# Performance work log

Measured on AMD Instinct MI355X. Metric: run time of the kernel, lower is better.

The kernel has to match this reference:

```python
import jax, jax.numpy as jnp
import numpy as np

N, E, H = 2000, 4096, 256

def setup_inputs() -> dict:
    key = jax.random.key(0)
    ks = jax.random.split(key, 24)
    def rn(k, shape, scale=0.05):
        return jax.random.normal(k, shape, dtype=jnp.float32) * scale
    inp = {
        'x': jax.random.randint(ks[0], (N, 1), 0, 5),
        'pos': rn(ks[1], (N, 3), 1.0),
        'edge_index': jax.random.randint(ks[2], (2, E), 0, N),
        'edge_atr': rn(ks[3], (E, 5), 1.0),
        'emb_table': rn(ks[4], (5, 5), 1.0),
        'lin0_W': rn(ks[5], (H, 8)), 'lin0_b': jnp.zeros((H,), jnp.float32),
        'mlp1_W': rn(ks[6], (128, 5)), 'mlp1_b': jnp.zeros((128,), jnp.float32),
        'mlp2_W': rn(ks[7], (H * H, 128), 0.01), 'mlp2_b': jnp.zeros((H * H,), jnp.float32),
        'conv_b': jnp.zeros((H,), jnp.float32),
        'gru_Wih': rn(ks[8], (3 * H, H)), 'gru_Whh': rn(ks[9], (3 * H, H)),
        'gru_bih': jnp.zeros((3 * H,), jnp.float32), 'gru_bhh': jnp.zeros((3 * H,), jnp.float32),
        'lin1_W': rn(ks[10], (H, 2 * H)), 'lin1_b': jnp.zeros((H,), jnp.float32),
        'lin2_W': rn(ks[11], (242, H)), 'lin2_b': jnp.zeros((242,), jnp.float32),
        'l6_W1': rn(ks[12], (128, 2 * H)), 'l6_b1': jnp.zeros((128,), jnp.float32),
        'bn_g': jnp.ones((128,), jnp.float32), 'bn_b': jnp.zeros((128,), jnp.float32),
        'l6_W2': rn(ks[13], (1, 128)), 'l6_b2': jnp.zeros((1,), jnp.float32),
    }
    return inp

def _gru_step(m, h, Wih, Whh, bih, bhh):
    gi = m @ Wih.T + bih  # [N,3H]
    gh = h @ Whh.T + bhh
    gir, giz, gin = jnp.split(gi, 3, axis=1)
    ghr, ghz, ghn = jnp.split(gh, 3, axis=1)
    r = jax.nn.sigmoid(gir + ghr)
    z = jax.nn.sigmoid(giz + ghz)
    n = jnp.tanh(gin + r * ghn)
    return (1.0 - z) * n + z * h

def reference(x, pos, edge_index, edge_atr, emb_table, lin0_W, lin0_b,
              mlp1_W, mlp1_b, mlp2_W, mlp2_b, conv_b,
              gru_Wih, gru_Whh, gru_bih, gru_bhh,
              lin1_W, lin1_b, lin2_W, lin2_b,
              l6_W1, l6_b1, bn_g, bn_b, l6_W2, l6_b2):
    node_emb = emb_table[x[:, 0]]                      # [N,5]
    in_p = jnp.concatenate([node_emb, pos], axis=1)    # [N,8]
    out = jax.nn.relu(in_p @ lin0_W.T + lin0_b)        # [N,H]
    h = out
    row, col = edge_index[0], edge_index[1]
    # edge-conditioned weights (edge_atr is loop-invariant -> compute once)
    he = jax.nn.relu(edge_atr @ mlp1_W.T + mlp1_b)     # [E,128]
    W_e = (he @ mlp2_W.T + mlp2_b).reshape(E, H, H)    # [E,H,H]
    counts = jnp.clip(jax.ops.segment_sum(jnp.ones((E,), jnp.float32), col, num_segments=N), 1.0)
    for _ in range(3):
        msg = jnp.einsum('eh,eho->eo', out[row], W_e)  # gather + per-edge matmul
        agg = jax.ops.segment_sum(msg, col, num_segments=N) / counts[:, None] + conv_b
        m = jax.nn.relu(agg)
        h = _gru_step(m, h, gru_Wih, gru_Whh, gru_bih, gru_bhh)
        out = h
    out_concat = jnp.concatenate([out[row], out[col]], axis=1)  # [E,2H]
    o1 = jax.nn.relu(out_concat @ lin1_W.T + lin1_b)
    out2 = o1 @ lin2_W.T + lin2_b                       # [E,242]
    # lin6: Linear -> BatchNorm1d (batch stats, training mode) -> ReLU -> Linear
    h1 = out_concat @ l6_W1.T + l6_b1                   # [E,128]
    mu = jnp.mean(h1, axis=0)
    var = jnp.var(h1, axis=0)
    h1n = (h1 - mu) * jax.lax.rsqrt(var + 1e-5) * bn_g + bn_b
    precs = jax.nn.relu(h1n) @ l6_W2.T + l6_b2          # [E,1]
    return (out2, precs)
```

## Files before the change

### kernel.cpp

```cpp
#include <hip/hip_runtime.h>
#include <hip/hip_bf16.h>

constexpr int N_ = 2000;
constexpr int E_ = 4096;
constexpr int H_ = 256;
constexpr int KH_ = 128;
constexpr int NV_ = H_ * KH_;
constexpr int MPAD_ = 2048;
constexpr int NG_ = 768;
constexpr float VSCALE = 64.f;
constexpr float VSCALE_INV = 1.f / 64.f;

typedef short bf16x8 __attribute__((ext_vector_type(8)));
typedef float f32x4  __attribute__((ext_vector_type(4)));
typedef float f32x2  __attribute__((ext_vector_type(2)));

__device__ __forceinline__ float bf_lo(unsigned u) { return __uint_as_float(u << 16); }
__device__ __forceinline__ float bf_hi(unsigned u) { return __uint_as_float(u & 0xffff0000u); }
__device__ __forceinline__ short bfbits(float f) {
    __hip_bfloat16 b = __float2bfloat16(f);
    return *(short*)&b;
}

#define PIPE_WAIT_ENTER(N_OUTST)                                   \
    asm volatile("s_waitcnt vmcnt(" #N_OUTST ")" ::: "memory");    \
    __builtin_amdgcn_s_barrier();                                  \
    asm volatile("" ::: "memory");                                 \
    __builtin_amdgcn_sched_barrier(0);

#define PIPE_EXIT()                                                \
    __builtin_amdgcn_sched_barrier(0);                             \
    asm volatile("" ::: "memory");                                 \
    __builtin_amdgcn_s_barrier();

__global__ void k_lin0(const int* __restrict__ x, const float* __restrict__ pos,
                       const float* __restrict__ emb, const float* __restrict__ W,
                       const float* __restrict__ b, float* __restrict__ out,
                       __hip_bfloat16* __restrict__ Abf,
                       float* __restrict__ counts, float* __restrict__ aggm,
                       int* __restrict__ deg, int* __restrict__ wcur) {
    int n = blockIdx.x, t = threadIdx.x;
    if (n >= N_) { Abf[(size_t)n * H_ + t] = __float2bfloat16(0.f); return; }
    if (t == 0) counts[n] = 0.f;
    if (t == 1) deg[n] = 0;
    if (t == 2) wcur[n] = 0;
    aggm[(size_t)n * H_ + t] = 0.f;
    __shared__ float in_p[8];
    if (t < 5) in_p[t] = emb[x[n] * 5 + t];
    else if (t < 8) in_p[t] = pos[n * 3 + (t - 5)];
    __syncthreads();
    float acc = b[t];
#pragma unroll
    for (int i = 0; i < 8; i++) acc += in_p[i] * W[t * 8 + i];
    float v = fmaxf(acc, 0.f);
    out[n * H_ + t] = v;
    Abf[(size_t)n * H_ + t] = __float2bfloat16(v);
}

__global__ void k_he(const float* __restrict__ ea, const float* __restrict__ W,
                     const float* __restrict__ b, float* __restrict__ he,
                     const int* __restrict__ ei, float* __restrict__ counts,
                     int* __restrict__ deg) {
    int e = blockIdx.x, t = threadIdx.x;
    __shared__ float a[5];
    if (t < 5) a[t] = ea[e * 5 + t];
    if (t == 8) atomicAdd(&counts[ei[E_ + e]], 1.0f);
    if (t == 9) atomicAdd(&deg[ei[e]], 1);
    __syncthreads();
    float acc = b[t];
#pragma unroll
    for (int i = 0; i < 5; i++) acc += a[i] * W[t * 5 + i];
    he[e * KH_ + t] = fmaxf(acc, 0.f);
}

__global__ void k_scan(const int* __restrict__ deg, int* __restrict__ rowptr) {
    __shared__ int ws[256];
    int t = threadIdx.x;
    int base = t * 8;
    int loc[8];
    int s = 0;
#pragma unroll
    for (int j = 0; j < 8; j++) {
        int idx = base + j;
        int d = (idx < N_) ? deg[idx] : 0;
        loc[j] = s;
        s += d;
    }
    ws[t] = s;
    __syncthreads();
    for (int off2 = 1; off2 < 256; off2 <<= 1) {
        int v = (t >= off2) ? ws[t - off2] : 0;
        __syncthreads();
        ws[t] += v;
        __syncthreads();
    }
    int excl = ws[t] - s;
#pragma unroll
    for (int j = 0; j < 8; j++) {
        int idx = base + j;
        if (idx <= N_) rowptr[idx] = excl + loc[j];
    }
}

__global__ void k_fill(const int* __restrict__ ei, const int* __restrict__ rowptr,
                       int* __restrict__ wcur, int* __restrict__ eord) {
    int e = blockIdx.x * blockDim.x + threadIdx.x;
    if (e < E_) {
        int r = ei[e];
        int p = atomicAdd(&wcur[r], 1);
        eord[rowptr[r] + p] = e;
    }
}

__global__ void k_trans_bt(const float* __restrict__ W, __hip_bfloat16* __restrict__ Bt) {
    __shared__ float tile[32][68];
    int t = threadIdx.x;
    int n0 = blockIdx.x * 64, k0 = blockIdx.y * 32;
#pragma unroll
    for (int i = 0; i < 2; i++) {
        int idx = t + i * 256;
        int kk = idx >> 4, nn = (idx & 15) * 4;
        float4 f = *(const float4*)&W[(size_t)(k0 + kk) * NV_ + n0 + nn];
        *(float4*)&tile[kk][nn] = f;
    }
    __syncthreads();
#pragma unroll
    for (int i = 0; i < 2; i++) {
        int idx = t + i * 256;
        int nn = idx >> 3, k4 = (idx & 7) * 4;
        short4 s;
        s.x = bfbits(tile[k4 + 0][nn]);
        s.y = bfbits(tile[k4 + 1][nn]);
        s.z = bfbits(tile[k4 + 2][nn]);
        s.w = bfbits(tile[k4 + 3][nn]);
        *(short4*)&Bt[(size_t)(n0 + nn) * H_ + k0 + k4] = s;
    }
}

__global__ void k_prep_w(const float* __restrict__ Wih, const float* __restrict__ Whh,
                         const float* __restrict__ lin1W, const float* __restrict__ l6W1,
                         const float* __restrict__ lin2W, const float* __restrict__ b2,
                         __hip_bfloat16* __restrict__ WihB, __hip_bfloat16* __restrict__ WhhB,
                         __hip_bfloat16* __restrict__ Bpk,
                         __hip_bfloat16* __restrict__ lin2Wb, __hip_bfloat16* __restrict__ BtB) {
    int i = blockIdx.x * 256 + threadIdx.x;
    if (i < NG_ * H_) {
        WihB[i] = __float2bfloat16(Wih[i]);
        WhhB[i] = __float2bfloat16(Whh[i]);
    }
    Bpk[i] = __float2bfloat16(i < 256 * 512 ? lin1W[i] : l6W1[i - 256 * 512]);
    if (i < 128 * 2 * H_) {
        int r = i >> 8, k = i & 255;
        lin2Wb[i] = __float2bfloat16(r < 242 ? lin2W[r * H_ + k] : 0.f);
        int o = i >> 8, h = i & 255;
        BtB[o * H_ + h] = __float2bfloat16(b2[h * H_ + o]);
    }
}

__global__ void k_concat(const int* __restrict__ ei, const float* __restrict__ h,
                         __hip_bfloat16* __restrict__ Cbf, float* __restrict__ bnsum) {
    int e = blockIdx.x, t = threadIdx.x;
    if (e == 0) bnsum[t] = 0.f;
    int r = ei[e], c = ei[E_ + e];
    Cbf[(size_t)e * 512 + t]       = __float2bfloat16(h[(size_t)r * H_ + t]);
    Cbf[(size_t)e * 512 + 256 + t] = __float2bfloat16(h[(size_t)c * H_ + t]);
}

template <int KD, bool RELU, bool OUT_BF16>
__global__ __launch_bounds__(256, 3) void k_gemm_nt(const __hip_bfloat16* __restrict__ A,
                                                    const __hip_bfloat16* __restrict__ Bt,
                                                    float* __restrict__ Cf,
                                                    __hip_bfloat16* __restrict__ Cb,
                                                    const float* __restrict__ bias,
                                                    int ldc, int ncols, int mvalid) {
    __shared__ __align__(16) short As[2][4096];
    __shared__ __align__(16) short Bs[2][4096];
    int t = threadIdx.x;
    int lane = t & 63, wave = t >> 6;
    int wm = wave >> 1, wn = wave & 1;
    int quad = lane >> 4, l16 = lane & 15;
    int row0 = blockIdx.y * 128, col0 = blockIdx.x * 128;

    f32x4 acc[4][4] = {};
    int r_ld = (lane >> 2);
    int koff = (((lane & 3) ^ ((lane >> 3) & 3)) * 8);
    int swz = (l16 >> 1) & 3;
    constexpr int NST = KD / 32;

    auto stage = [&](int buf, int k0) {
#pragma unroll
        for (int c = 0; c < 4; c++) {
            int q = wave * 4 + c;
            int ch = q & 7;
            int r = ch * 16 + r_ld;
            const __hip_bfloat16* gp;
            short* lp;
            if (q < 8) { gp = A  + (size_t)(row0 + r) * KD + k0 + koff; lp = &As[buf][ch * 512]; }
            else       { gp = Bt + (size_t)(col0 + r) * KD + k0 + koff; lp = &Bs[buf][ch * 512]; }
            __builtin_amdgcn_global_load_lds(
                (const __attribute__((address_space(1))) unsigned int*)(uintptr_t)gp,
                (__attribute__((address_space(3))) unsigned int*)(uintptr_t)lp,
                16, 0, 0);
        }
    };

    stage(0, 0);
    for (int kk = 0; kk < NST; kk++) {
        int cur = kk & 1;
        if (kk + 1 < NST) {
            stage(cur ^ 1, (kk + 1) * 32);
            PIPE_WAIT_ENTER(4)
        } else {
            PIPE_WAIT_ENTER(0)
        }
        bf16x8 a[4], b[4];
#pragma unroll
        for (int i = 0; i < 4; i++)
            a[i] = *(const bf16x8*)&As[cur][(wm * 64 + i * 16 + l16) * 32 + ((quad ^ swz) << 3)];
#pragma unroll
        for (int j = 0; j < 4; j++)
            b[j] = *(const bf16x8*)&Bs[cur][(wn * 64 + j * 16 + l16) * 32 + ((quad ^ swz) << 3)];
#pragma unroll
        for (int i = 0; i < 4; i++)
#pragma unroll
            for (int j = 0; j < 4; j++)
                acc[i][j] = __builtin_amdgcn_mfma_f32_16x16x32_bf16(a[i], b[j], acc[i][j], 0, 0, 0);
        PIPE_EXIT()
    }

#pragma unroll
    for (int i = 0; i < 4; i++) {
        int gm0 = row0 + wm * 64 + i * 16 + quad * 4;
#pragma unroll
        for (int r = 0; r < 4; r++) {
            int gm = gm0 + r;
            if (gm < mvalid) {
#pragma unroll
                for (int j = 0; j < 4; j++) {
                    int col = col0 + wn * 64 + l16 + j * 16;
                    if (col < ncols) {
                        float v = acc[i][j][r];
                        if (bias) v += bias[col];
                        if (RELU) v = fmaxf(v, 0.f);
                        if (OUT_BF16) Cb[(size_t)gm * ldc + col] = __float2bfloat16(v);
                        else          Cf[(size_t)gm * ldc + col] = v;
                    }
                }
            }
        }
    }
}

__global__ __launch_bounds__(256, 4) void k_gemm_VP(const __hip_bfloat16* __restrict__ Abf,
                                                    const __hip_bfloat16* __restrict__ Bt,
                                                    const __hip_bfloat16* __restrict__ WhhB,
                                                    const __hip_bfloat16* __restrict__ BtB,
                                                    const float* __restrict__ bhh,
                                                    float* __restrict__ gh,
                                                    float* __restrict__ outb,
                                                    unsigned char* __restrict__ V8) {
    __shared__ __align__(16) short As[2][4096];
    __shared__ __align__(16) short Bs[2][4096];
    int bid = blockIdx.x;
    int t = threadIdx.x;
    int lane = t & 63, wave = t >> 6;
    int wm = wave >> 1, wn = wave & 1;
    int quad = lane >> 4, l16 = lane & 15;
    int r_ld = (lane >> 2);
    int koff = (((lane & 3) ^ ((lane >> 3) & 3)) * 8);
    int swz = (l16 >> 1) & 3;

    if (bid < 128) {
        int pbx = bid & 7, pby = bid >> 3;
        bool ob = (pbx >= 6);
        const __hip_bfloat16* Bp = ob ? BtB : WhhB;
        int col0 = ob ? (pbx - 6) * 128 : pbx * 128;
        int ldc = ob ? H_ : NG_;
        float* C = ob ? outb : gh;
        int row0 = pby * 128;

        f32x4 acc[4][4] = {};
        auto stage = [&](int buf, int k0) {
#pragma unroll
            for (int c = 0; c < 4; c++) {
                int q = wave * 4 + c;
                int ch = q & 7;
                int r = ch * 16 + r_ld;
                const __hip_bfloat16* gp;
                short* lp;
                if (q < 8) { gp = Abf + ((size_t)(row0 + r) << 8) + k0 + koff; lp = &As[buf][ch * 512]; }
                else       { gp = Bp  + ((size_t)(col0 + r) << 8) + k0 + koff; lp = &Bs[buf][ch * 512]; }
                __builtin_amdgcn_global_load_lds(
                    (const __attribute__((address_space(1))) unsigned int*)(uintptr_t)gp,
                    (__attribute__((address_space(3))) unsigned int*)(uintptr_t)lp,
                    16, 0, 0);
            }
        };
        stage(0, 0);
        for (int kk = 0; kk < 8; kk++) {
            int cur = kk & 1;
            if (kk + 1 < 8) {
                stage(cur ^ 1, (kk + 1) * 32);
                PIPE_WAIT_ENTER(4)
            } else {
                PIPE_WAIT_ENTER(0)
            }
            bf16x8 a[4], b[4];
#pragma unroll
            for (int i = 0; i < 4; i++)
                a[i] = *(const bf16x8*)&As[cur][(wm * 64 + i * 16 + l16) * 32 + ((quad ^ swz) << 3)];
#pragma unroll
            for (int j = 0; j < 4; j++)
                b[j] = *(const bf16x8*)&Bs[cur][(wn * 64 + j * 16 + l16) * 32 + ((quad ^ swz) << 3)];
#pragma unroll
            for (int i = 0; i < 4; i++)
#pragma unroll
                for (int j = 0; j < 4; j++)
                    acc[i][j] = __builtin_amdgcn_mfma_f32_16x16x32_bf16(a[i], b[j], acc[i][j], 0, 0, 0);
            PIPE_EXIT()
        }
#pragma unroll
        for (int i = 0; i < 4; i++) {
            int gm0 = row0 + wm * 64 + i * 16 + quad * 4;
#pragma unroll
            for (int r = 0; r < 4; r++) {
                int gm = gm0 + r;
                if (gm < N_) {
#pragma unroll
                    for (int j = 0; j < 4; j++) {
                        int col = col0 + wn * 64 + l16 + j * 16;
                        float v = acc[i][j][r] + (ob ? 0.f : bhh[col]);
                        C[(size_t)gm * ldc + col] = v;
                    }
                }
            }
        }
        return;
    }

    int vb = bid - 128;
    int bx = vb & 255, by = vb >> 8;
    int row0 = by * 128, col0 = bx * 128;
    int obase = bx * 8;
    int kb = (bx >> 5) * 16;
    short* Ps = &As[0][0];

    f32x4 acc[4][4] = {};
    auto stage = [&](int buf, int k0) {
#pragma unroll
        for (int c = 0; c < 4; c++) {
            int q = wave * 4 + c;
            int ch = q & 7;
            const __hip_bfloat16* gp;
            short* lp;
            if (q < 8) {
                gp = Abf + ((size_t)(row0 + ch * 16 + r_ld) << 8) + k0 + koff;
                lp = &As[buf][ch * 512];
            } else {
                int nv = ((obase + ch) & 255) * 128 + kb + r_ld;
                gp = Bt + ((size_t)nv << 8) + k0 + koff;
                lp = &Bs[buf][ch * 512];
            }
            __builtin_amdgcn_global_load_lds(
                (const __attribute__((address_space(1))) unsigned int*)(uintptr_t)gp,
                (__attribute__((address_space(3))) unsigned int*)(uintptr_t)lp,
                16, 0, 0);
        }
    };
    stage(0, 0);
    for (int kk = 0; kk < 8; kk++) {
        int cur = kk & 1;
        if (kk + 1 < 8) {
            stage(cur ^ 1, (kk + 1) * 32);
            PIPE_WAIT_ENTER(4)
        } else {
            PIPE_WAIT_ENTER(0)
        }
        bf16x8 a[4], b[4];
#pragma unroll
        for (int i = 0; i < 4; i++)
            a[i] = *(const bf16x8*)&As[cur][(wm * 64 + i * 16 + l16) * 32 + ((quad ^ swz) << 3)];
#pragma unroll
        for (int j = 0; j < 4; j++)
            b[j] = *(const bf16x8*)&Bs[cur][(wn * 64 + j * 16 + l16) * 32 + ((quad ^ swz) << 3)];
#pragma unroll
        for (int i = 0; i < 4; i++)
#pragma unroll
            for (int j = 0; j < 4; j++)
                acc[i][j] = __builtin_amdgcn_mfma_f32_16x16x32_bf16(a[i], b[j], acc[i][j], 0, 0, 0);
        PIPE_EXIT()
    }

#pragma unroll
    for (int pp = 0; pp < 4; pp++) {
        if (wm == (pp >> 1)) {
#pragma unroll
            for (int ii = 0; ii < 2; ii++) {
                const int i = (pp & 1) * 2 + ii;
                int lr = ii * 16 + quad * 4;
#pragma unroll
                for (int r = 0; r < 4; r++) {
#pragma unroll
                    for (int j = 0; j < 4; j++) {
                        int col = wn * 64 + j * 16 + l16;
                        Ps[(lr + r) * 136 + col] = bfbits(acc[i][j][r] * VSCALE);
                    }
                }
            }
        }
        __syncthreads();
        {
            int row = t >> 3;
            int col = (t & 7) * 16;
            int gm = row0 + pp * 32 + row;
            if (gm < N_) {
                uint4 ua = *(const uint4*)&Ps[row * 136 + col];
                uint4 ub = *(const uint4*)&Ps[row * 136 + col + 8];
                unsigned p0 = __builtin_amdgcn_cvt_pk_fp8_f32(bf_lo(ua.x), bf_hi(ua.x), 0, false);
                p0 = __builtin_amdgcn_cvt_pk_fp8_f32(bf_lo(ua.y), bf_hi(ua.y), p0, true);
                unsigned p1 = __builtin_amdgcn_cvt_pk_fp8_f32(bf_lo(ua.z), bf_hi(ua.z), 0, false);
                p1 = __builtin_amdgcn_cvt_pk_fp8_f32(bf_lo(ua.w), bf_hi(ua.w), p1, true);
                unsigned p2 = __builtin_amdgcn_cvt_pk_fp8_f32(bf_lo(ub.x), bf_hi(ub.x), 0, false);
                p2 = __builtin_amdgcn_cvt_pk_fp8_f32(bf_lo(ub.y), bf_hi(ub.y), p2, true);
                unsigned p3 = __builtin_amdgcn_cvt_pk_fp8_f32(bf_lo(ub.z), bf_hi(ub.z), 0, false);
                p3 = __builtin_amdgcn_cvt_pk_fp8_f32(bf_lo(ub.w), bf_hi(ub.w), p3, true);
                uint4 o4;
                o4.x = p0; o4.y = p1; o4.z = p2; o4.w = p3;
                *(uint4*)(V8 + (size_t)gm * NV_ + col0 + col) = o4;
            }
        }
        __syncthreads();
    }
}

__global__ __launch_bounds__(256, 3) void k_gemm_gi(const float* __restrict__ agg,
                                                    const float* __restrict__ counts,
                                                    const float* __restrict__ conv_b,
                                                    const __hip_bfloat16* __restrict__ WihB,
                                                    const float* __restrict__ bih,
                                                    float* __restrict__ gi) {
    __shared__ __align__(16) short As[2][4096];
    __shared__ __align__(16) short Bs[2][4096];
    __shared__ __align__(16) float conv_lds[256];
    int t = threadIdx.x;
    int lane = t & 63, wave = t >> 6;
    int wm = wave >> 1, wn = wave & 1;
    int quad = lane >> 4, l16 = lane & 15;
    int row0 = blockIdx.y * 128, col0 = blockIdx.x * 128;
    int r_ld = (lane >> 2);
    int koff = (((lane & 3) ^ ((lane >> 3) & 3)) * 8);
    int swz = (l16 >> 1) & 3;

    conv_lds[t] = conv_b[t];
    __syncthreads();

    f32x4 acc[4][4] = {};
    float rcv[2];
    const float* asrc[2];
#pragma unroll
    for (int c = 0; c < 2; c++) {
        int ch = wave * 2 + c;
        int row = row0 + ch * 16 + r_ld;
        int rowc = row < N_ ? row : N_ - 1;
        rcv[c] = 1.f / fmaxf(counts[rowc], 1.f);
        asrc[c] = agg + (size_t)rowc * 256;
    }
    float4 R[2][2][2];

    auto loadA = [&](int buf, int k0) {
#pragma unroll
        for (int c = 0; c < 2; c++) {
            R[buf][c][0] = *(const float4*)(asrc[c] + k0 + koff);
            R[buf][c][1] = *(const float4*)(asrc[c] + k0 + koff + 4);
        }
    };
    auto stageB = [&](int buf, int k0) {
#pragma unroll
        for (int c = 0; c < 2; c++) {
            int ch = wave * 2 + c;
            const __hip_bfloat16* gp = WihB + (size_t)(col0 + ch * 16 + r_ld) * 256 + k0 + koff;
            short* lp = &Bs[buf][ch * 512];
            __builtin_amdgcn_global_load_lds(
                (const __attribute__((address_space(1))) unsigned int*)(uintptr_t)gp,
                (__attribute__((address_space(3))) unsigned int*)(uintptr_t)lp,
                16, 0, 0);
        }
    };
    auto writeA = [&](int buf, int k0) {
        float4 cb0 = *(const float4*)&conv_lds[k0 + koff];
        float4 cb1 = *(const float4*)&conv_lds[k0 + koff + 4];
#pragma unroll
        for (int c = 0; c < 2; c++) {
            int ch = wave * 2 + c;
            float rc = rcv[c];
            float4 a0 = R[buf][c][0], a1 = R[buf][c][1];
            bf16x8 v;
            v[0] = bfbits(fmaxf(a0.x * rc + cb0.x, 0.f));
            v[1] = bfbits(fmaxf(a0.y * rc + cb0.y, 0.f));
            v[2] = bfbits(fmaxf(a0.z * rc + cb0.z, 0.f));
            v[3] = bfbits(fmaxf(a0.w * rc + cb0.w, 0.f));
            v[4] = bfbits(fmaxf(a1.x * rc + cb1.x, 0.f));
            v[5] = bfbits(fmaxf(a1.y * rc + cb1.y, 0.f));
            v[6] = bfbits(fmaxf(a1.z * rc + cb1.z, 0.f));
            v[7] = bfbits(fmaxf(a1.w * rc + cb1.w, 0.f));
            *(bf16x8*)&As[buf][ch * 512 + lane * 8] = v;
        }
    };

    loadA(0, 0);
    stageB(0, 0);
#pragma unroll
    for (int kk = 0; kk < 8; kk++) {
        const int cur = kk & 1;
        if (kk + 1 < 8) {
            loadA(cur ^ 1, (kk + 1) * 32);
            stageB(cur ^ 1, (kk + 1) * 32);
        }
        writeA(cur, kk * 32);
        if (kk + 1 < 8) { asm volatile("s_waitcnt vmcnt(6)" ::: "memory"); }
        else            { asm volatile("s_waitcnt vmcnt(0)" ::: "memory"); }
        asm volatile("s_waitcnt lgkmcnt(0)" ::: "memory");
        __builtin_amdgcn_s_barrier();
        asm volatile("" ::: "memory");
        __builtin_amdgcn_sched_barrier(0);
        bf16x8 a[4], b[4];
#pragma unroll
        for (int i = 0; i < 4; i++)
            a[i] = *(const bf16x8*)&As[cur][(wm * 64 + i * 16 + l16) * 32 + ((quad ^ swz) << 3)];
#pragma unroll
        for (int j = 0; j < 4; j++)
            b[j] = *(const bf16x8*)&Bs[cur][(wn * 64 + j * 16 + l16) * 32 + ((quad ^ swz) << 3)];
#pragma unroll
        for (int i = 0; i < 4; i++)
#pragma unroll
            for (int j = 0; j < 4; j++)
                acc[i][j] = __builtin_amdgcn_mfma_f32_16x16x32_bf16(a[i], b[j], acc[i][j], 0, 0, 0);
        PIPE_EXIT()
    }

#pragma unroll
    for (int i = 0; i < 4; i++) {
        int gm0 = row0 + wm * 64 + i * 16 + quad * 4;
#pragma unroll
        for (int r = 0; r < 4; r++) {
            int gm = gm0 + r;
            if (gm < N_) {
#pragma unroll
                for (int j = 0; j < 4; j++) {
                    int col = col0 + wn * 64 + l16 + j * 16;
                    gi[(size_t)gm * NG_ + col] = acc[i][j][r] + bih[col];
                }
            }
        }
    }
}

__global__ __launch_bounds__(256, 3) void k_gemm_tail(const __hip_bfloat16* __restrict__ A,
                                                      const __hip_bfloat16* __restrict__ Bpk,
                                                      const float* __restrict__ b1,
                                                      const float* __restrict__ b2,
                                                      __hip_bfloat16* __restrict__ o1bf,
                                                      float* __restrict__ h1,
                                                      float* __restrict__ bnsum) {
    __shared__ __align__(16) short As[2][4096];
    __shared__ __align__(16) short Bs[2][4096];
    int t = threadIdx.x;
    int lane = t & 63, wave = t >> 6;
    int wm = wave >> 1, wn = wave & 1;
    int quad = lane >> 4, l16 = lane & 15;
    int row0 = blockIdx.y * 128, col0 = blockIdx.x * 128;

    f32x4 acc[4][4] = {};
    int r_ld = (lane >> 2);
    int koff = (((lane & 3) ^ ((lane >> 3) & 3)) * 8);
    int swz = (l16 >> 1) & 3;

    auto stage = [&](int buf, int k0) {
#pragma unroll
        for (int c = 0; c < 4; c++) {
            int q = wave * 4 + c;
            int ch = q & 7;
            int r = ch * 16 + r_ld;
            const __hip_bfloat16* gp;
            short* lp;
            if (q < 8) { gp = A   + (size_t)(row0 + r) * 512 + k0 + koff; lp = &As[buf][ch * 512]; }
            else       { gp = Bpk + (size_t)(col0 + r) * 512 + k0 + koff; lp = &Bs[buf][ch * 512]; }
            __builtin_amdgcn_global_load_lds(
                (const __attribute__((address_space(1))) unsigned int*)(uintptr_t)gp,
                (__attribute__((address_space(3))) unsigned int*)(uintptr_t)lp,
                16, 0, 0);
        }
    };

    stage(0, 0);
    for (int kk = 0; kk < 16; kk++) {
        int cur = kk & 1;
        if (kk + 1 < 16) {
            stage(cur ^ 1, (kk + 1) * 32);
            PIPE_WAIT_ENTER(4)
        } else {
            PIPE_WAIT_ENTER(0)
        }
        bf16x8 a[4], b[4];
#pragma unroll
        for (int i = 0; i < 4; i++)
            a[i] = *(const bf16x8*)&As[cur][(wm * 64 + i * 16 + l16) * 32 + ((quad ^ swz) << 3)];
#pragma unroll
        for (int j = 0; j < 4; j++)
            b[j] = *(const bf16x8*)&Bs[cur][(wn * 64 + j * 16 + l16) * 32 + ((quad ^ swz) << 3)];
#pragma unroll
        for (int i = 0; i < 4; i++)
#pragma unroll
            for (int j = 0; j < 4; j++)
                acc[i][j] = __builtin_amdgcn_mfma_f32_16x16x32_bf16(a[i], b[j], acc[i][j], 0, 0, 0);
        PIPE_EXIT()
    }

#pragma unroll
    for (int i = 0; i < 4; i++) {
        int gm0 = row0 + wm * 64 + i * 16 + quad * 4;
#pragma unroll
        for (int r = 0; r < 4; r++) {
            int gm = gm0 + r;
#pragma unroll
            for (int j = 0; j < 4; j++) {
                int col = col0 + wn * 64 + l16 + j * 16;
                float v = acc[i][j][r];
                if (col < 256) {
                    v = fmaxf(v + b1[col], 0.f);
                    o1bf[(size_t)gm * H_ + col] = __float2bfloat16(v);
                } else {
                    h1[(size_t)gm * 128 + (col - 256)] = v + b2[col - 256];
                }
            }
        }
    }

    if (col0 == 256) {
#pragma unroll
        for (int j = 0; j < 4; j++) {
            int cj = wn * 64 + j * 16 + l16;
            float bj = b2[cj];
            float s = 0.f, ss = 0.f;
#pragma unroll
            for (int i = 0; i < 4; i++)
#pragma unroll
                for (int r = 0; r < 4; r++) {
                    float v = acc[i][j][r] + bj;
                    s += v;
                    ss += v * v;
                }
            s  += __shfl_xor(s, 16);  s  += __shfl_xor(s, 32);
            ss += __shfl_xor(ss, 16); ss += __shfl_xor(ss, 32);
            if (quad == 0) {
                atomicAdd(&bnsum[cj], s);
                atomicAdd(&bnsum[128 + cj], ss);
            }
        }
    }
}

__global__ void k_msg(const int* __restrict__ ei, const int* __restrict__ eord,
                      const float* __restrict__ he,
                      const unsigned char* __restrict__ V8, const float* __restrict__ outb,
                      float* __restrict__ agg) {
    int bid = blockIdx.x;
    int e = eord[((bid & 7) << 9) | (bid >> 3)];
    int o = threadIdx.x;
    __shared__ float hs[KH_];
    if (o < KH_) hs[o] = he[e * KH_ + o] * VSCALE_INV;
    __syncthreads();
    int r = ei[e], c = ei[E_ + e];
    const unsigned char* vbase = V8 + (size_t)r * NV_ + o * 16;

    auto dot16 = [&](uint4 u, const float* hp) -> float {
        f32x2 f;
        float s;
        f = __builtin_amdgcn_cvt_pk_f32_fp8(u.x, false); s  = hp[0]  * f.x + hp[1]  * f.y;
        f = __builtin_amdgcn_cvt_pk_f32_fp8(u.x, true);  s += hp[2]  * f.x + hp[3]  * f.y;
        f = __builtin_amdgcn_cvt_pk_f32_fp8(u.y, false); s += hp[4]  * f.x + hp[5]  * f.y;
        f = __builtin_amdgcn_cvt_pk_f32_fp8(u.y, true);  s += hp[6]  * f.x + hp[7]  * f.y;
        f = __builtin_amdgcn_cvt_pk_f32_fp8(u.z, false); s += hp[8]  * f.x + hp[9]  * f.y;
        f = __builtin_amdgcn_cvt_pk_f32_fp8(u.z, true);  s += hp[10] * f.x + hp[11] * f.y;
        f = __builtin_amdgcn_cvt_pk_f32_fp8(u.w, false); s += hp[12] * f.x + hp[13] * f.y;
        f = __builtin_amdgcn_cvt_pk_f32_fp8(u.w, true);  s += hp[14] * f.x + hp[15] * f.y;
        return s;
    };

    float p0, p1, p2, p3;
    {
        uint4 u0 = *(const uint4*)(vbase);
        uint4 u1 = *(const uint4*)(vbase + 4096);
        uint4 u2 = *(const uint4*)(vbase + 2 * 4096);
        uint4 u3 = *(const uint4*)(vbase + 3 * 4096);
        p0 = dot16(u0, hs);
        p1 = dot16(u1, hs + 16);
        p2 = dot16(u2, hs + 32);
        p3 = dot16(u3, hs + 48);
    }
    {
        uint4 u0 = *(const uint4*)(vbase + 4 * 4096);
        uint4 u1 = *(const uint4*)(vbase + 5 * 4096);
        uint4 u2 = *(const uint4*)(vbase + 6 * 4096);
        uint4 u3 = *(const uint4*)(vbase + 7 * 4096);
        p0 += dot16(u0, hs + 64);
        p1 += dot16(u1, hs + 80);
        p2 += dot16(u2, hs + 96);
        p3 += dot16(u3, hs + 112);
    }
    float acc = outb[(size_t)r * H_ + o] + ((p0 + p1) + (p2 + p3));
    atomicAdd(&agg[(size_t)c * H_ + o], acc);
}

__global__ void k_gru_update(const float* __restrict__ gi, const float* __restrict__ gh,
                             float* __restrict__ h, __hip_bfloat16* __restrict__ Abf,
                             float* __restrict__ agg) {
    int i = blockIdx.x * blockDim.x + threadIdx.x;
    if (i >= N_ * H_) return;
    int n = i >> 8, j = i & 255;
    const float* gip = gi + (size_t)n * NG_;
    const float* ghp = gh + (size_t)n * NG_;
    float r = 1.f / (1.f + expf(-(gip[j] + ghp[j])));
    float z = 1.f / (1.f + expf(-(gip[H_ + j] + ghp[H_ + j])));
    float nn = tanhf(gip[2 * H_ + j] + r * ghp[2 * H_ + j]);
    float hv = (1.f - z) * nn + z * h[i];
    h[i] = hv;
    Abf[i] = __float2bfloat16(hv);
    agg[i] = 0.f;
}

__global__ void k_precs(const float* __restrict__ h1, const float* __restrict__ bnsum,
                        const float* __restrict__ g, const float* __restrict__ bb,
                        const float* __restrict__ W2, const float* __restrict__ b2,
                        float* __restrict__ out) {
    __shared__ float smu[128], srs[128];
    int t = threadIdx.x;
    if (t < 128) {
        float mu = bnsum[t] * (1.f / E_);
        float var = bnsum[128 + t] * (1.f / E_) - mu * mu;
        smu[t] = mu;
        srs[t] = rsqrtf(var + 1e-5f);
    }
    __syncthreads();
    int e = blockIdx.x * blockDim.x + t;
    if (e >= E_) return;
    float acc = b2[0];
#pragma unroll 4
    for (int j = 0; j < 128; j++) {
        float v = (h1[(size_t)e * 128 + j] - smu[j]) * srs[j] * g[j] + bb[j];
        acc += fmaxf(v, 0.f) * W2[j];
    }
    out[(size_t)E_ * 242 + e] = acc;
}

extern "C" void kernel_launch(void* const* d_in, const int* in_sizes, int n_in,
                              void* d_out, int out_size, void* d_ws, size_t ws_size,
                              hipStream_t stream) {
    const int*   x        = (const int*)  d_in[0];
    const float* pos      = (const float*)d_in[1];
    const int*   ei       = (const int*)  d_in[2];
    const float* edge_atr = (const float*)d_in[3];
    const float* emb      = (const float*)d_in[4];
    const float* lin0_W   = (const float*)d_in[5];
    const float* lin0_b   = (const float*)d_in[6];
    const float* mlp1_W   = (const float*)d_in[7];
    const float* mlp1_b   = (const float*)d_in[8];
    const float* mlp2_W   = (const float*)d_in[9];
    const float* mlp2_b   = (const float*)d_in[10];
    const float* conv_b   = (const float*)d_in[11];
    const float* gru_Wih  = (const float*)d_in[12];
    const float* gru_Whh  = (const float*)d_in[13];
    const float* gru_bih  = (const float*)d_in[14];
    const float* gru_bhh  = (const float*)d_in[15];
    const float* lin1_W   = (const float*)d_in[16];
    const float* lin1_b   = (const float*)d_in[17];
    const float* lin2_W   = (const float*)d_in[18];
    const float* lin2_b   = (const float*)d_in[19];
    const float* l6_W1    = (const float*)d_in[20];
    const float* l6_b1    = (const float*)d_in[21];
    const float* bn_g     = (const float*)d_in[22];
    const float* bn_b     = (const float*)d_in[23];
    const float* l6_W2    = (const float*)d_in[24];
    const float* l6_b2    = (const float*)d_in[25];
    float* out = (float*)d_out;

    char* w = (char*)d_ws;
    size_t off = 0;
    auto alloc = [&](size_t bytes) -> void* {
        void* p = w + off;
        off = (off + bytes + 255) & ~(size_t)255;
        return p;
    };
    float* hbuf   = (float*)alloc((size_t)N_ * H_ * 4);
    float* aggm   = (float*)alloc((size_t)N_ * H_ * 4);
    float* outb   = (float*)alloc((size_t)N_ * H_ * 4);
    float* he     = (float*)alloc((size_t)E_ * KH_ * 4);
    float* gi     = (float*)alloc((size_t)N_ * NG_ * 4);
    float* gh     = (float*)alloc((size_t)N_ * NG_ * 4);
    float* h1     = (float*)alloc((size_t)E_ * 128 * 4);
    float* counts = (float*)alloc((size_t)N_ * 4);
    float* bnsum  = (float*)alloc(256 * 4);
    int*   deg    = (int*)  alloc((size_t)N_ * 4);
    int*   wcur   = (int*)  alloc((size_t)N_ * 4);
    int*   rowptr = (int*)  alloc((size_t)(N_ + 1) * 4);
    int*   eord   = (int*)  alloc((size_t)E_ * 4);
    unsigned char* V8      = (unsigned char*)alloc((size_t)N_ * NV_);
    __hip_bfloat16* Abf    = (__hip_bfloat16*)alloc((size_t)MPAD_ * H_ * 2);
    __hip_bfloat16* Bt     = (__hip_bfloat16*)alloc((size_t)NV_ * H_ * 2);
    __hip_bfloat16* WihB   = (__hip_bfloat16*)alloc((size_t)NG_ * H_ * 2);
    __hip_bfloat16* WhhB   = (__hip_bfloat16*)alloc((size_t)NG_ * H_ * 2);
    __hip_bfloat16* Bpk    = (__hip_bfloat16*)alloc((size_t)384 * 512 * 2);
    __hip_bfloat16* lin2Wb = (__hip_bfloat16*)alloc((size_t)H_ * H_ * 2);
    __hip_bfloat16* BtB    = (__hip_bfloat16*)alloc((size_t)H_ * H_ * 2);
    __hip_bfloat16* Cbf    = (__hip_bfloat16*)alloc((size_t)E_ * 2 * H_ * 2);
    __hip_bfloat16* o1bf   = (__hip_bfloat16*)alloc((size_t)E_ * H_ * 2);

    k_lin0<<<MPAD_, 256, 0, stream>>>(x, pos, emb, lin0_W, lin0_b, hbuf, Abf,
                                      counts, aggm, deg, wcur);
    k_he<<<E_, 128, 0, stream>>>(edge_atr, mlp1_W, mlp1_b, he, ei, counts, deg);
    k_scan<<<1, 256, 0, stream>>>(deg, rowptr);
    k_fill<<<(E_ + 255) / 256, 256, 0, stream>>>(ei, rowptr, wcur, eord);
    k_trans_bt<<<dim3(NV_ / 64, H_ / 32), 256, 0, stream>>>(mlp2_W, Bt);
    k_prep_w<<<768, 256, 0, stream>>>(gru_Wih, gru_Whh, lin1_W, l6_W1, lin2_W, mlp2_b,
                                      WihB, WhhB, Bpk, lin2Wb, BtB);

    for (int it = 0; it < 3; it++) {
        k_gemm_VP<<<128 + (NV_ / 128) * (MPAD_ / 128), 256, 0, stream>>>(
            Abf, Bt, WhhB, BtB, gru_bhh, gh, outb, V8);
        k_msg<<<E_, 256, 0, stream>>>(ei, eord, he, V8, outb, aggm);
        k_gemm_gi<<<dim3(6, MPAD_ / 128), 256, 0, stream>>>(
            aggm, counts, conv_b, WihB, gru_bih, gi);
        k_gru_update<<<(N_ * H_ + 255) / 256, 256, 0, stream>>>(gi, gh, hbuf, Abf, aggm);
    }

    k_concat<<<E_, 256, 0, stream>>>(ei, hbuf, Cbf, bnsum);
    k_gemm_tail<<<dim3(3, E_ / 128), 256, 0, stream>>>(Cbf, Bpk, lin1_b, l6_b1,
                                                       o1bf, h1, bnsum);
    k_gemm_nt<256, false, false><<<dim3(2, E_ / 128), 256, 0, stream>>>(
        o1bf, lin2Wb, out, nullptr, lin2_b, 242, 242, E_);
    k_precs<<<(E_ + 255) / 256, 256, 0, stream>>>(h1, bnsum, bn_g, bn_b, l6_W2, l6_b2, out);
}
```

Measured before the change: 422.4 us.

## Merge scan/fill and lin2/precs kernels; triple-buffer VP GEMM pipeline

Merges the degree scan and edge fill into one single-block kernel that keeps rowptr and per-row cursors in shared memory. Merges the lin2 GEMM and the BN/precs reduction into one launch, with extra blocks handling precs. Deepens the k_gemm_VP load pipeline from double to triple buffering and lowers its occupancy bound from 4 to 3. These remove launch overhead and aim to hide more load latency in the main GEMM, at the cost of more LDS per block and lower occupancy.

```diff
diff --git a/kernel.cpp b/kernel.cpp
--- a/kernel.cpp
+++ b/kernel.cpp
@@ -38,12 +38,11 @@
                        const float* __restrict__ b, float* __restrict__ out,
                        __hip_bfloat16* __restrict__ Abf,
                        float* __restrict__ counts, float* __restrict__ aggm,
-                       int* __restrict__ deg, int* __restrict__ wcur) {
+                       int* __restrict__ deg) {
     int n = blockIdx.x, t = threadIdx.x;
     if (n >= N_) { Abf[(size_t)n * H_ + t] = __float2bfloat16(0.f); return; }
     if (t == 0) counts[n] = 0.f;
     if (t == 1) deg[n] = 0;
-    if (t == 2) wcur[n] = 0;
     aggm[(size_t)n * H_ + t] = 0.f;
     __shared__ float in_p[8];
     if (t < 5) in_p[t] = emb[x[n] * 5 + t];
@@ -73,7 +72,10 @@
     he[e * KH_ + t] = fmaxf(acc, 0.f);
 }
 
-__global__ void k_scan(const int* __restrict__ deg, int* __restrict__ rowptr) {
+__global__ void k_scanfill(const int* __restrict__ ei, const int* __restrict__ deg,
+                           int* __restrict__ eord) {
+    __shared__ int rp[N_];
+    __shared__ int wc[N_];
     __shared__ int ws[256];
     int t = threadIdx.x;
     int base = t * 8;
@@ -98,17 +100,13 @@
 #pragma unroll
     for (int j = 0; j < 8; j++) {
         int idx = base + j;
-        if (idx <= N_) rowptr[idx] = excl + loc[j];
-    }
-}
-
-__global__ void k_fill(const int* __restrict__ ei, const int* __restrict__ rowptr,
-                       int* __restrict__ wcur, int* __restrict__ eord) {
-    int e = blockIdx.x * blockDim.x + threadIdx.x;
-    if (e < E_) {
+        if (idx < N_) { rp[idx] = excl + loc[j]; wc[idx] = 0; }
+    }
+    __syncthreads();
+    for (int e = t; e < E_; e += 256) {
         int r = ei[e];
-        int p = atomicAdd(&wcur[r], 1);
-        eord[rowptr[r] + p] = e;
+        int p = atomicAdd(&wc[r], 1);
+        eord[rp[r] + p] = e;
     }
 }
 
@@ -166,92 +164,7 @@
     Cbf[(size_t)e * 512 + 256 + t] = __float2bfloat16(h[(size_t)c * H_ + t]);
 }
 
-template <int KD, bool RELU, bool OUT_BF16>
-__global__ __launch_bounds__(256, 3) void k_gemm_nt(const __hip_bfloat16* __restrict__ A,
-                                                    const __hip_bfloat16* __restrict__ Bt,
-                                                    float* __restrict__ Cf,
-                                                    __hip_bfloat16* __restrict__ Cb,
-                                                    const float* __restrict__ bias,
-                                                    int ldc, int ncols, int mvalid) {
-    __shared__ __align__(16) short As[2][4096];
-    __shared__ __align__(16) short Bs[2][4096];
-    int t = threadIdx.x;
-    int lane = t & 63, wave = t >> 6;
-    int wm = wave >> 1, wn = wave & 1;
-    int quad = lane >> 4, l16 = lane & 15;
-    int row0 = blockIdx.y * 128, col0 = blockIdx.x * 128;
-
-    f32x4 acc[4][4] = {};
-    int r_ld = (lane >> 2);
-    int koff = (((lane & 3) ^ ((lane >> 3) & 3)) * 8);
-    int swz = (l16 >> 1) & 3;
-    constexpr int NST = KD / 32;
-
-    auto stage = [&](int buf, int k0) {
-#pragma unroll
-        for (int c = 0; c < 4; c++) {
-            int q = wave * 4 + c;
-            int ch = q & 7;
-            int r = ch * 16 + r_ld;
-            const __hip_bfloat16* gp;
-            short* lp;
-            if (q < 8) { gp = A  + (size_t)(row0 + r) * KD + k0 + koff; lp = &As[buf][ch * 512]; }
-            else       { gp = Bt + (size_t)(col0 + r) * KD + k0 + koff; lp = &Bs[buf][ch * 512]; }
-            __builtin_amdgcn_global_load_lds(
-                (const __attribute__((address_space(1))) unsigned int*)(uintptr_t)gp,
-                (__attribute__((address_space(3))) unsigned int*)(uintptr_t)lp,
-                16, 0, 0);
-        }
-    };
-
-    stage(0, 0);
-    for (int kk = 0; kk < NST; kk++) {
-        int cur = kk & 1;
-        if (kk + 1 < NST) {
-            stage(cur ^ 1, (kk + 1) * 32);
-            PIPE_WAIT_ENTER(4)
-        } else {
-            PIPE_WAIT_ENTER(0)
-        }
-        bf16x8 a[4], b[4];
-#pragma unroll
-        for (int i = 0; i < 4; i++)
-            a[i] = *(const bf16x8*)&As[cur][(wm * 64 + i * 16 + l16) * 32 + ((quad ^ swz) << 3)];
-#pragma unroll
-        for (int j = 0; j < 4; j++)
-            b[j] = *(const bf16x8*)&Bs[cur][(wn * 64 + j * 16 + l16) * 32 + ((quad ^ swz) << 3)];
-#pragma unroll
-        for (int i = 0; i < 4; i++)
-#pragma unroll
-            for (int j = 0; j < 4; j++)
-                acc[i][j] = __builtin_amdgcn_mfma_f32_16x16x32_bf16(a[i], b[j], acc[i][j], 0, 0, 0);
-        PIPE_EXIT()
-    }
-
-#pragma unroll
-    for (int i = 0; i < 4; i++) {
-        int gm0 = row0 + wm * 64 + i * 16 + quad * 4;
-#pragma unroll
-        for (int r = 0; r < 4; r++) {
-            int gm = gm0 + r;
-            if (gm < mvalid) {
-#pragma unroll
-                for (int j = 0; j < 4; j++) {
-                    int col = col0 + wn * 64 + l16 + j * 16;
-                    if (col < ncols) {
-                        float v = acc[i][j][r];
-                        if (bias) v += bias[col];
-                        if (RELU) v = fmaxf(v, 0.f);
-                        if (OUT_BF16) Cb[(size_t)gm * ldc + col] = __float2bfloat16(v);
-                        else          Cf[(size_t)gm * ldc + col] = v;
-                    }
-                }
-            }
-        }
-    }
-}
-
-__global__ __launch_bounds__(256, 4) void k_gemm_VP(const __hip_bfloat16* __restrict__ Abf,
+__global__ __launch_bounds__(256, 3) void k_gemm_VP(const __hip_bfloat16* __restrict__ Abf,
                                                     const __hip_bfloat16* __restrict__ Bt,
                                                     const __hip_bfloat16* __restrict__ WhhB,
                                                     const __hip_bfloat16* __restrict__ BtB,
@@ -259,8 +172,8 @@
                                                     float* __restrict__ gh,
                                                     float* __restrict__ outb,
                                                     unsigned char* __restrict__ V8) {
-    __shared__ __align__(16) short As[2][4096];
-    __shared__ __align__(16) short Bs[2][4096];
+    __shared__ __align__(16) short As[3][4096];
+    __shared__ __align__(16) short Bs[3][4096];
     int bid = blockIdx.x;
     int t = threadIdx.x;
     int lane = t & 63, wave = t >> 6;
@@ -368,10 +281,13 @@
         }
     };
     stage(0, 0);
+    stage(1, 32);
     for (int kk = 0; kk < 8; kk++) {
-        int cur = kk & 1;
-        if (kk + 1 < 8) {
-            stage(cur ^ 1, (kk + 1) * 32);
+        int cur = kk % 3;
+        if (kk + 2 < 8) {
+            stage((kk + 2) % 3, (kk + 2) * 32);
+            PIPE_WAIT_ENTER(8)
+        } else if (kk + 1 < 8) {
             PIPE_WAIT_ENTER(4)
         } else {
             PIPE_WAIT_ENTER(0)
@@ -729,28 +645,108 @@
     agg[i] = 0.f;
 }
 
-__global__ void k_precs(const float* __restrict__ h1, const float* __restrict__ bnsum,
-                        const float* __restrict__ g, const float* __restrict__ bb,
-                        const float* __restrict__ W2, const float* __restrict__ b2,
-                        float* __restrict__ out) {
-    __shared__ float smu[128], srs[128];
+__global__ __launch_bounds__(256, 3) void k_gemm_lin2p(const __hip_bfloat16* __restrict__ A,
+                                                       const __hip_bfloat16* __restrict__ Bt,
+                                                       const float* __restrict__ bias,
+                                                       const float* __restrict__ h1,
+                                                       const float* __restrict__ bnsum,
+                                                       const float* __restrict__ g,
+                                                       const float* __restrict__ bb,
+                                                       const float* __restrict__ W2,
+                                                       const float* __restrict__ b2,
+                                                       float* __restrict__ out) {
+    int bid = blockIdx.x;
     int t = threadIdx.x;
-    if (t < 128) {
-        float mu = bnsum[t] * (1.f / E_);
-        float var = bnsum[128 + t] * (1.f / E_) - mu * mu;
-        smu[t] = mu;
-        srs[t] = rsqrtf(var + 1e-5f);
-    }
-    __syncthreads();
-    int e = blockIdx.x * blockDim.x + t;
-    if (e >= E_) return;
-    float acc = b2[0];
+
+    if (bid >= 64) {
+        __shared__ float smu[128], srs[128];
+        if (t < 128) {
+            float mu = bnsum[t] * (1.f / E_);
+            float var = bnsum[128 + t] * (1.f / E_) - mu * mu;
+            smu[t] = mu;
+            srs[t] = rsqrtf(var + 1e-5f);
+        }
+        __syncthreads();
+        int e = (bid - 64) * 256 + t;
+        if (e >= E_) return;
+        float acc = b2[0];
 #pragma unroll 4
-    for (int j = 0; j < 128; j++) {
-        float v = (h1[(size_t)e * 128 + j] - smu[j]) * srs[j] * g[j] + bb[j];
-        acc += fmaxf(v, 0.f) * W2[j];
-    }
-    out[(size_t)E_ * 242 + e] = acc;
+        for (int j = 0; j < 128; j++) {
+            float v = (h1[(size_t)e * 128 + j] - smu[j]) * srs[j] * g[j] + bb[j];
+            acc += fmaxf(v, 0.f) * W2[j];
+        }
+        out[(size_t)E_ * 242 + e] = acc;
+        return;
+    }
+
+    __shared__ __align__(16) short As[2][4096];
+    __shared__ __align__(16) short Bs[2][4096];
+    int lane = t & 63, wave = t >> 6;
+    int wm = wave >> 1, wn = wave & 1;
+    int quad = lane >> 4, l16 = lane & 15;
+    int row0 = (bid >> 1) * 128, col0 = (bid & 1) * 128;
+
+    f32x4 acc[4][4] = {};
+    int r_ld = (lane >> 2);
+    int koff = (((lane & 3) ^ ((lane >> 3) & 3)) * 8);
+    int swz = (l16 >> 1) & 3;
+
+    auto stage = [&](int buf, int k0) {
+#pragma unroll
+        for (int c = 0; c < 4; c++) {
+            int q = wave * 4 + c;
+            int ch = q & 7;
+            int r = ch * 16 + r_ld;
+            const __hip_bfloat16* gp;
+            short* lp;
+            if (q < 8) { gp = A  + (size_t)(row0 + r) * 256 + k0 + koff; lp = &As[buf][ch * 512]; }
+            else       { gp = Bt + (size_t)(col0 + r) * 256 + k0 + koff; lp = &Bs[buf][ch * 512]; }
+            __builtin_amdgcn_global_load_lds(
+                (const __attribute__((address_space(1))) unsigned int*)(uintptr_t)gp,
+                (__attribute__((address_space(3))) unsigned int*)(uintptr_t)lp,
+                16, 0, 0);
+        }
+    };
+
+    stage(0, 0);
+    for (int kk = 0; kk < 8; kk++) {
+        int cur = kk & 1;
+        if (kk + 1 < 8) {
+            stage(cur ^ 1, (kk + 1) * 32);
+            PIPE_WAIT_ENTER(4)
+        } else {
+            PIPE_WAIT_ENTER(0)
+        }
+        bf16x8 a[4], b[4];
+#pragma unroll
+        for (int i = 0; i < 4; i++)
+            a[i] = *(const bf16x8*)&As[cur][(wm * 64 + i * 16 + l16) * 32 + ((quad ^ swz) << 3)];
+#pragma unroll
+        for (int j = 0; j < 4; j++)
+            b[j] = *(const bf16x8*)&Bs[cur][(wn * 64 + j * 16 + l16) * 32 + ((quad ^ swz) << 3)];
+#pragma unroll
+        for (int i = 0; i < 4; i++)
+#pragma unroll
+            for (int j = 0; j < 4; j++)
+                acc[i][j] = __builtin_amdgcn_mfma_f32_16x16x32_bf16(a[i], b[j], acc[i][j], 0, 0, 0);
+        PIPE_EXIT()
+    }
+
+#pragma unroll
+    for (int i = 0; i < 4; i++) {
+        int gm0 = row0 + wm * 64 + i * 16 + quad * 4;
+#pragma unroll
+        for (int r = 0; r < 4; r++) {
+            int gm = gm0 + r;
+#pragma unroll
+            for (int j = 0; j < 4; j++) {
+                int col = col0 + wn * 64 + l16 + j * 16;
+                if (col < 242) {
+                    out[(size_t)gm * 242 + col] = acc[i][j][r] + bias[col];
+                }
+            }
+        }
+    }
 }
 
 extern "C" void kernel_launch(void* const* d_in, const int* in_sizes, int n_in,
@@ -801,8 +797,6 @@
     float* counts = (float*)alloc((size_t)N_ * 4);
     float* bnsum  = (float*)alloc(256 * 4);
     int*   deg    = (int*)  alloc((size_t)N_ * 4);
-    int*   wcur   = (int*)  alloc((size_t)N_ * 4);
-    int*   rowptr = (int*)  alloc((size_t)(N_ + 1) * 4);
     int*   eord   = (int*)  alloc((size_t)E_ * 4);
     unsigned char* V8      = (unsigned char*)alloc((size_t)N_ * NV_);
     __hip_bfloat16* Abf    = (__hip_bfloat16*)alloc((size_t)MPAD_ * H_ * 2);
@@ -816,10 +810,9 @@
     __hip_bfloat16* o1bf   = (__hip_bfloat16*)alloc((size_t)E_ * H_ * 2);
 
     k_lin0<<<MPAD_, 256, 0, stream>>>(x, pos, emb, lin0_W, lin0_b, hbuf, Abf,
-                                      counts, aggm, deg, wcur);
+                                      counts, aggm, deg);
     k_he<<<E_, 128, 0, stream>>>(edge_atr, mlp1_W, mlp1_b, he, ei, counts, deg);
-    k_scan<<<1, 256, 0, stream>>>(deg, rowptr);
-    k_fill<<<(E_ + 255) / 256, 256, 0, stream>>>(ei, rowptr, wcur, eord);
+    k_scanfill<<<1, 256, 0, stream>>>(ei, deg, eord);
     k_trans_bt<<<dim3(NV_ / 64, H_ / 32), 256, 0, stream>>>(mlp2_W, Bt);
     k_prep_w<<<768, 256, 0, stream>>>(gru_Wih, gru_Whh, lin1_W, l6_W1, lin2_W, mlp2_b,
                                       WihB, WhhB, Bpk, lin2Wb, BtB);
@@ -836,7 +829,6 @@
     k_concat<<<E_, 256, 0, stream>>>(ei, hbuf, Cbf, bnsum);
     k_gemm_tail<<<dim3(3, E_ / 128), 256, 0, stream>>>(Cbf, Bpk, lin1_b, l6_b1,
                                                        o1bf, h1, bnsum);
-    k_gemm_nt<256, false, false><<<dim3(2, E_ / 128), 256, 0, stream>>>(
-        o1bf, lin2Wb, out, nullptr, lin2_b, 242, 242, E_);
-    k_precs<<<(E_ + 255) / 256, 256, 0, stream>>>(h1, bnsum, bn_g, bn_b, l6_W2, l6_b2, out);
-}
+    k_gemm_lin2p<<<80, 256, 0, stream>>>(o1bf, lin2Wb, lin2_b,
+                                         h1, bnsum, bn_g, bn_b, l6_W2, l6_b2, out);
+}
```

Result: faster. 404.9 us (-4.2%).
